# Kernel tuning notes

Measured on AMD Instinct MI355X. Metric: run time of the kernel, lower is better.

The kernel has to match this reference:

```python
import jax, jax.numpy as jnp
import numpy as np

BLOCK, HALO, HEADS, DH = 8, 4, 4, 32
EPS = 1e-5


def _convT(x, w, p):
    # torch ConvTranspose2d(stride=1, padding=p) == conv with flipped/transposed kernel, padding k-1-p
    k = w.shape[-1]
    w2 = jnp.flip(w, axis=(-2, -1)).transpose(1, 0, 2, 3)  # (Cin,Cout,k,k) -> (Cout,Cin,k,k)
    pad = k - 1 - p
    return jax.lax.conv_general_dilated(x, w2, (1, 1), ((pad, pad), (pad, pad)),
                                        dimension_numbers=('NCHW', 'OIHW', 'NCHW'))


def _bn(x, g, b, m, v):
    s = g * jax.lax.rsqrt(v + EPS)
    return x * s[None, :, None, None] + (b - m * s)[None, :, None, None]


def _rel_to_abs(x):
    # x: [b, l, 2r-1] -> [b, l, r]
    b, l, m = x.shape
    r = (m + 1) // 2
    x = jnp.concatenate([x, jnp.zeros((b, l, 1), x.dtype)], axis=2)
    flat = jnp.concatenate([x.reshape(b, l * (m + 1)), jnp.zeros((b, m - l), x.dtype)], axis=1)
    return flat.reshape(b, l + 1, m)[:, :l, -r:]


def _rel_logits_1d(q, rel_k):
    # q: [b, x, y, d]; rel_k: [2r-1, d] -> [b, x, r, y, r]
    b, x, y, d = q.shape
    r = (rel_k.shape[0] + 1) // 2
    logits = jnp.einsum('bxyd,rd->bxyr', q, rel_k)
    logits = _rel_to_abs(logits.reshape(b * x, y, -1)).reshape(b, x, y, r)
    return jnp.broadcast_to(logits[:, :, None, :, :], (b, x, r, y, r))


def _rel_pos_emb(q, rel_h, rel_w):
    # q: [bb, block*block, dh] (already scaled, per halonet-pytorch)
    bb, n, d = q.shape
    qg = q.reshape(bb, BLOCK, BLOCK, d)
    lw = _rel_logits_1d(qg, rel_w).transpose(0, 1, 3, 2, 4).reshape(bb, n, -1)  # b (x y) (i j)
    lh = _rel_logits_1d(qg.transpose(0, 2, 1, 3), rel_h).transpose(0, 3, 1, 4, 2).reshape(bb, n, -1)  # b (y x) (j i)
    return lw + lh


def _halo_attn(x, to_q, to_kv, to_out_w, to_out_b, rel_h, rel_w):
    B, C, H, W = x.shape
    b, h = BLOCK, HALO
    nh, nw = H // b, W // b
    nblk = nh * nw
    wsz = b + 2 * h
    inner = to_q.shape[1]
    scale = DH ** -0.5
    # queries: non-overlapping blocks -> [B*nblk, b*b, C]
    q_inp = x.reshape(B, C, nh, b, nw, b).transpose(0, 2, 4, 3, 5, 1).reshape(B * nblk, b * b, C)
    # keys/values: overlapping halo windows (F.unfold) -> [B*nblk, wsz*wsz, C]
    pat = jax.lax.conv_general_dilated_patches(x, (wsz, wsz), (b, b), ((h, h), (h, h)))  # [B, C*wsz*wsz, nh, nw]
    kv_inp = pat.reshape(B, C, wsz * wsz, nblk).transpose(0, 3, 2, 1).reshape(B * nblk, wsz * wsz, C)
    q = q_inp @ to_q
    k, v = jnp.split(kv_inp @ to_kv, 2, axis=-1)
    def heads(t):
        return t.reshape(t.shape[0], t.shape[1], HEADS, DH).transpose(0, 2, 1, 3).reshape(-1, t.shape[1], DH)
    q, k, v = heads(q) * scale, heads(k), heads(v)
    sim = jnp.einsum('bid,bjd->bij', q, k) + _rel_pos_emb(q, rel_h, rel_w)  # [B*nblk*HEADS, b*b, wsz*wsz]
    # mask out halo positions that fall into zero padding
    ones = jnp.ones((1, 1, H, W), x.dtype)
    mpat = jax.lax.conv_general_dilated_patches(ones, (wsz, wsz), (b, b), ((h, h), (h, h)))
    mask = mpat.reshape(wsz * wsz, nblk).T > 0  # [nblk, wsz*wsz]
    neg = -jnp.finfo(sim.dtype).max
    sim = jnp.where(mask[None, :, None, None, :],
                    sim.reshape(B, nblk, HEADS, b * b, wsz * wsz), neg)
    attn = jax.nn.softmax(sim, axis=-1).reshape(-1, b * b, wsz * wsz)
    out = jnp.einsum('bij,bjd->bid', attn, v)
    out = out.reshape(B * nblk, HEADS, b * b, DH).transpose(0, 2, 1, 3).reshape(B * nblk, b * b, inner)
    out = out @ to_out_w + to_out_b
    return out.reshape(B, nh, nw, b, b, C).transpose(0, 5, 1, 3, 2, 4).reshape(B, C, H, W)


def setup_inputs() -> dict:
    key = jax.random.key(0)
    ks = jax.random.split(key, 13)
    B, C, H, W = 2, 128, 192, 192
    inner = HEADS * DH
    rel = 2 * (BLOCK + 2 * HALO) - 1  # 31
    n = lambda k, s, sc: jax.random.normal(k, s, jnp.float32) * sc
    return {
        'x': jax.random.normal(ks[0], (B, C, H, W), jnp.float32),
        'conv1_w': n(ks[1], (C, C, 1, 1), 0.1),
        'bn1_g': jnp.ones((C,), jnp.float32), 'bn1_b': jnp.zeros((C,), jnp.float32),
        'bn1_m': n(ks[2], (C,), 0.1),
        'bn1_v': jax.random.uniform(ks[3], (C,), jnp.float32, 0.5, 1.5),
        'to_q': n(ks[4], (C, inner), 0.05), 'to_kv': n(ks[5], (C, 2 * inner), 0.05),
        'to_out_w': n(ks[6], (inner, C), 0.05), 'to_out_b': n(ks[7], (C,), 0.01),
        'rel_h': n(ks[8], (rel, DH), DH ** -0.5), 'rel_w': n(ks[9], (rel, DH), DH ** -0.5),
        'conv3_w': n(ks[10], (C, C, 3, 3), 0.05),
        'bn3_g': jnp.ones((C,), jnp.float32), 'bn3_b': jnp.zeros((C,), jnp.float32),
        'bn3_m': n(ks[11], (C,), 0.1),
        'bn3_v': jax.random.uniform(ks[12], (C,), jnp.float32, 0.5, 1.5),
    }


def reference(x, conv1_w, bn1_g, bn1_b, bn1_m, bn1_v, to_q, to_kv, to_out_w, to_out_b,
              rel_h, rel_w, conv3_w, bn3_g, bn3_b, bn3_m, bn3_v):
    # Bottleneck (stride=1, no downsample): conv1x1T -> BN -> ReLU -> HaloAttention -> ReLU
    #   -> conv3x3T -> BN -> +identity -> ReLU
    out = jax.nn.relu(_bn(_convT(x, conv1_w, 0), bn1_g, bn1_b, bn1_m, bn1_v))
    out = jax.nn.relu(_halo_attn(out, to_q, to_kv, to_out_w, to_out_b, rel_h, rel_w))
    out = _bn(_convT(out, conv3_w, 1), bn3_g, bn3_b, bn3_m, bn3_v)
    return jax.nn.relu(out + x)
```

## Files before the change

kernel.cpp:

```cpp
#include <hip/hip_runtime.h>
#include <hip/hip_bf16.h>

using bf16 = __hip_bfloat16;
typedef unsigned short u16;
typedef unsigned int   u32;
typedef __attribute__((ext_vector_type(8))) short short8;
typedef __attribute__((ext_vector_type(4))) float f32x4;

#define B_N 2
#define CCH 128
#define HH 192
#define WW 192
#define HWS (HH*WW)
#define NPIX (B_N*HWS)
#define NBLKS 576
#define EPSV 1e-5f
#define LDW 136

__device__ __forceinline__ float b2f(bf16 v){ return __bfloat162float(v); }
__device__ __forceinline__ bf16  f2b(float v){ return __float2bfloat16(v); }
__device__ __forceinline__ u16  bits(bf16 v){ return *(u16*)&v; }
__device__ __forceinline__ float lo16(u32 u){ union{u32 i; float f;} x; x.i = u << 16;        return x.f; }
__device__ __forceinline__ float hi16(u32 u){ union{u32 i; float f;} x; x.i = u & 0xffff0000u; return x.f; }
__device__ __forceinline__ u32 pck(float a, float b){
    bf16 x = f2b(a), y = f2b(b);
    return (u32)*(u16*)&x | ((u32)*(u16*)&y << 16);
}

__global__ __launch_bounds__(256) void transpose_in(const float* __restrict__ x,
                                                    bf16* __restrict__ xT)
{
    __shared__ float tile[128][17];
    const int t   = threadIdx.x;
    const int hw0 = blockIdx.x * 16;
    const int n   = hw0 / HWS;
    const int hwl = hw0 - n*HWS;
    const int px = t & 15, cb = t >> 4;
    #pragma unroll
    for (int r = 0; r < 8; ++r){
        int ci = r*16 + cb;
        tile[ci][px] = x[(size_t)(n*CCH + ci)*HWS + hwl + px];
    }
    __syncthreads();
    const int pix = t >> 4, cig = t & 15;
    uint4 pk;
    pk.x = pck(tile[cig*8+0][pix], tile[cig*8+1][pix]);
    pk.y = pck(tile[cig*8+2][pix], tile[cig*8+3][pix]);
    pk.z = pck(tile[cig*8+4][pix], tile[cig*8+5][pix]);
    pk.w = pck(tile[cig*8+6][pix], tile[cig*8+7][pix]);
    *(uint4*)&xT[(size_t)(hw0 + pix)*CCH + cig*8] = pk;
}

__global__ __launch_bounds__(256) void prep_w(
    const float* __restrict__ w1, const float* __restrict__ to_q,
    const float* __restrict__ to_kv, const float* __restrict__ to_ow,
    const float* __restrict__ w3, bf16* __restrict__ wb)
{
    int i = blockIdx.x*256 + threadIdx.x;
    float v;
    if (i < 16384){       int co=(i>>7)&127, ci=i&127;      v = w1[ci*128+co]; }
    else if (i < 32768){  int r=i-16384; int co=r>>7, ci=r&127; v = to_q[ci*128+co]*0.17677669529663687f; }
    else if (i < 49152){  int r=i-32768; int co=r>>7, ci=r&127; v = to_kv[ci*256+co]; }
    else if (i < 65536){  int r=i-49152; int co=r>>7, ci=r&127; v = to_kv[ci*256+128+co]; }
    else if (i < 81920){  int r=i-65536; int co=r>>7, ci=r&127; v = to_ow[ci*128+co]; }
    else { int r=i-81920; int tap=r>>14, co=(r>>7)&127, ci=r&127; int a=tap/3, b=tap-a*3;
           v = w3[((size_t)(ci*128+co)*3+a)*3+b]; }
    wb[i] = f2b(v);
}

template<bool DO_BN, bool DO_BIAS, bool DO_RELU>
__global__ __launch_bounds__(256) void gemm_mfma(
    const bf16* __restrict__ inp, const bf16* __restrict__ Wp,
    bf16* __restrict__ outp, int cstride, int choff,
    const float* __restrict__ bn_g, const float* __restrict__ bn_b,
    const float* __restrict__ bn_m, const float* __restrict__ bn_v,
    const float* __restrict__ bias)
{
    Wp    += (size_t)blockIdx.y * 16384;
    choff += blockIdx.y * 128;
    __shared__ u16 sW[128*LDW];
    __shared__ u16 sX[64*LDW];
    const int tid  = threadIdx.x;
    const int pix0 = blockIdx.x * 64;
    const int lane = tid & 63;
    const int ln = lane & 15, g = lane >> 4;
    const int cow = (tid >> 6) * 32;

    #pragma unroll
    for (int r = 0; r < 8; ++r){
        int e = tid + r*256; int row = e>>4, grp = e&15;
        *(uint4*)&sW[row*LDW + grp*8] = *(const uint4*)&Wp[row*128 + grp*8];
    }
    #pragma unroll
    for (int r = 0; r < 4; ++r){
        int e = tid + r*256; int row = e>>4, grp = e&15;
        *(uint4*)&sX[row*LDW + grp*8] = *(const uint4*)&inp[(size_t)(pix0+row)*CCH + grp*8];
    }
    __syncthreads();

    f32x4 acc[4][2];
    #pragma unroll
    for (int mi=0;mi<4;mi++)
        #pragma unroll
        for (int ni=0;ni<2;ni++) acc[mi][ni] = (f32x4){0.f,0.f,0.f,0.f};

    #pragma unroll
    for (int kk = 0; kk < 4; ++kk){
        short8 fa[4], fb[2];
        #pragma unroll
        for (int mi=0;mi<4;mi++)
            fa[mi] = *(const short8*)&sX[(mi*16+ln)*LDW + kk*32 + g*8];
        #pragma unroll
        for (int ni=0;ni<2;ni++)
            fb[ni] = *(const short8*)&sW[(cow+ni*16+ln)*LDW + kk*32 + g*8];
        #pragma unroll
        for (int mi=0;mi<4;mi++)
            #pragma unroll
            for (int ni=0;ni<2;ni++)
                acc[mi][ni] = __builtin_amdgcn_mfma_f32_16x16x32_bf16(fa[mi], fb[ni], acc[mi][ni], 0, 0, 0);
    }

    float sc[2], bb[2];
    #pragma unroll
    for (int ni=0;ni<2;ni++){
        int co = cow + ni*16 + ln;
        sc[ni] = 1.f; bb[ni] = 0.f;
        if (DO_BN){ float sg = bn_g[co]*rsqrtf(bn_v[co]+EPSV); sc[ni]=sg; bb[ni]=bn_b[co]-bn_m[co]*sg; }
        if (DO_BIAS) bb[ni] += bias[co];
    }
    #pragma unroll
    for (int mi=0;mi<4;mi++)
        #pragma unroll
        for (int ni=0;ni<2;ni++)
            #pragma unroll
            for (int j=0;j<4;j++){
                int pix = pix0 + mi*16 + g*4 + j;
                int co  = cow + ni*16 + ln;
                float v = acc[mi][ni][j]*sc[ni] + bb[ni];
                if (DO_RELU) v = fmaxf(v, 0.f);
                outp[(size_t)pix*cstride + choff + co] = f2b(v);
            }
}

__global__ __launch_bounds__(256) void conv3_mfma(
    const bf16* __restrict__ inp, const bf16* __restrict__ W3p,
    const float* __restrict__ xin, float* __restrict__ outp,
    const float* __restrict__ g3, const float* __restrict__ b3,
    const float* __restrict__ m3, const float* __restrict__ v3)
{
    __shared__ u16 sW[128*LDW];
    __shared__ u16 sX[64*LDW];
    const int tid = threadIdx.x;
    const int P0  = blockIdx.x * 64;
    const int n   = P0 / HWS;
    const int hwb = P0 - n*HWS;
    const int h = hwb / WW, wb = hwb - h*WW;
    const int lane = tid & 63, ln = lane & 15, g = lane >> 4;
    const int cow = (tid >> 6) * 32;

    f32x4 acc[2][4];
    #pragma unroll
    for (int mi=0;mi<2;mi++)
        #pragma unroll
        for (int ni=0;ni<4;ni++) acc[mi][ni] = (f32x4){0.f,0.f,0.f,0.f};

    for (int tap = 0; tap < 9; ++tap){
        const int a = tap/3, b = tap - a*3;
        const int hs = h + 1 - a;
        if (hs < 0 || hs >= HH) continue;
        const int ws0 = wb + 1 - b;
        __syncthreads();
        #pragma unroll
        for (int r = 0; r < 8; ++r){
            int e = tid + r*256; int row = e>>4, grp = e&15;
            *(uint4*)&sW[row*LDW + grp*8] = *(const uint4*)&W3p[tap*16384 + row*128 + grp*8];
        }
        #pragma unroll
        for (int r = 0; r < 4; ++r){
            int e = tid + r*256; int row = e>>4, grp = e&15;
            int wsrc = ws0 + row;
            uint4 val = {0u,0u,0u,0u};
            if (wsrc >= 0 && wsrc < WW)
                val = *(const uint4*)&inp[(size_t)(n*HWS + hs*WW + wsrc)*CCH + grp*8];
            *(uint4*)&sX[row*LDW + grp*8] = val;
        }
        __syncthreads();
        #pragma unroll
        for (int kk = 0; kk < 4; ++kk){
            short8 fa[2], fb[4];
            #pragma unroll
            for (int mi=0;mi<2;mi++)
                fa[mi] = *(const short8*)&sW[(cow+mi*16+ln)*LDW + kk*32 + g*8];
            #pragma unroll
            for (int ni=0;ni<4;ni++)
                fb[ni] = *(const short8*)&sX[(ni*16+ln)*LDW + kk*32 + g*8];
            #pragma unroll
            for (int mi=0;mi<2;mi++)
                #pragma unroll
                for (int ni=0;ni<4;ni++)
                    acc[mi][ni] = __builtin_amdgcn_mfma_f32_16x16x32_bf16(fa[mi], fb[ni], acc[mi][ni], 0, 0, 0);
        }
    }

    #pragma unroll
    for (int mi=0;mi<2;mi++)
        #pragma unroll
        for (int j=0;j<4;j++){
            int co = cow + mi*16 + g*4 + j;
            float sg = g3[co]*rsqrtf(v3[co]+EPSV);
            float bc = b3[co] - m3[co]*sg;
            #pragma unroll
            for (int ni=0;ni<4;ni++){
                int pixl = hwb + ni*16 + ln;
                size_t idx = (size_t)(n*CCH + co)*HWS + pixl;
                float v = acc[mi][ni][j]*sg + bc + xin[idx];
                outp[idx] = fmaxf(v, 0.f);
            }
        }
}

__global__ __launch_bounds__(512) void attn_kernel(
    const bf16* __restrict__ QKV, const float* __restrict__ relh,
    const float* __restrict__ relw, bf16* __restrict__ outp)
{
    __shared__ __align__(16) char smem[60160];
    u16*   sQb  = (u16*)(smem);
    u16*   sK   = (u16*)(smem + 5120);
    u16*   sRH  = (u16*)(smem + 25600);
    u16*   sRW  = (u16*)(smem + 28160);
    u16*   sP   = (u16*)(smem);
    u16*   sVT  = (u16*)(smem + 33792);
    float* tT   = (float*)(smem + 50688);
    float* wredM= (float*)(smem + 59136);
    float* wredS= (float*)(smem + 59648);

    const int tid  = threadIdx.x;
    const int bid  = blockIdx.x;
    const int head = bid & 3;
    const int t    = bid >> 2;
    const int n    = t / NBLKS;
    const int blk  = t - n*NBLKS;
    const int bi = blk / 24, bj = blk - bi*24;
    const int row0 = bi*8 - 4, col0 = bj*8 - 4;
    const int ch0 = head*32;
    const int wv = tid >> 6, lane = tid & 63, ln = lane & 15, g = lane >> 4;
    const int nt = wv & 3, mh = wv >> 2;

    for (int e = tid; e < 1024; e += 512){
        int r = e >> 5, d = e & 31;
        u16 vh = 0, vw = 0;
        if (r < 31){ vh = bits(f2b(relh[r*32+d])); vw = bits(f2b(relw[r*32+d])); }
        sRH[r*40 + d] = vh;
        sRW[r*40 + d] = vw;
    }
    {
        int qq = tid >> 3, db = tid & 7;
        size_t P = (size_t)n*HWS + (bi*8 + (qq>>3))*WW + bj*8 + (qq&7);
        *(uint2*)&sQb[qq*40 + db*4] = *(const uint2*)&QKV[P*384 + ch0 + db*4];
    }
    #pragma unroll
    for (int r = 0; r < 4; ++r){
        int e = tid + r*512;
        int wp = e >> 3, db = e & 7;
        int rr = row0 + (wp>>4), cc2 = col0 + (wp&15);
        uint2 kk = {0u,0u}, vv = {0u,0u};
        if (rr>=0 && rr<HH && cc2>=0 && cc2<WW){
            size_t P = (size_t)n*HWS + rr*WW + cc2;
            kk = *(const uint2*)&QKV[P*384 + 128 + ch0 + db*4];
            vv = *(const uint2*)&QKV[P*384 + 256 + ch0 + db*4];
        }
        *(uint2*)&sK[wp*40 + db*4] = kk;
        sVT[(db*4+0)*264 + wp] = (u16)(vv.x & 0xffff);
        sVT[(db*4+1)*264 + wp] = (u16)(vv.x >> 16);
        sVT[(db*4+2)*264 + wp] = (u16)(vv.y & 0xffff);
        sVT[(db*4+3)*264 + wp] = (u16)(vv.y >> 16);
    }
    __syncthreads();

    const short8 qfrag = *(const short8*)&sQb[(nt*16+ln)*40 + g*8];
    f32x4 accs[8];
    #pragma unroll
    for (int i=0;i<8;i++){
        short8 fk = *(const short8*)&sK[((mh*8+i)*16+ln)*40 + g*8];
        accs[i] = __builtin_amdgcn_mfma_f32_16x16x32_bf16(fk, qfrag, (f32x4){0.f,0.f,0.f,0.f}, 0, 0, 0);
    }

    {
        const u16* sRX = mh ? sRW : sRH;
        #pragma unroll
        for (int ntr=0; ntr<2; ++ntr){
            short8 fr = *(const short8*)&sRX[(ntr*16+ln)*40 + g*8];
            f32x4 L = __builtin_amdgcn_mfma_f32_16x16x32_bf16(qfrag, fr, (f32x4){0.f,0.f,0.f,0.f}, 0, 0, 0);
            #pragma unroll
            for (int r2=0;r2<4;r2++){
                int q  = nt*16 + g*4 + r2;
                int rr = ntr*16 + ln;
                int bq = mh ? (q&7) : (q>>3);
                int iw = rr - 15 + bq;
                if (iw >= 0 && iw < 16) tT[mh*1056 + iw*66 + q] = L[r2];
            }
        }
    }
    __syncthreads();

    const int qc = nt*16 + ln;
    float tw[4];
    bool cok[4];
    #pragma unroll
    for (int r2=0;r2<4;r2++){
        tw[r2] = tT[1056 + (g*4+r2)*66 + qc];
        int cc2 = col0 + g*4 + r2;
        cok[r2] = (cc2 >= 0 && cc2 < WW);
    }
    float mx = -3.4e38f;
    #pragma unroll
    for (int i=0;i<8;i++){
        int mt = mh*8 + i;
        int rr = row0 + mt;
        bool rok = (rr >= 0 && rr < HH);
        float th = tT[mt*66 + qc];
        #pragma unroll
        for (int r2=0;r2<4;r2++){
            float s = (rok && cok[r2]) ? (accs[i][r2] + th + tw[r2]) : -3.0e38f;
            accs[i][r2] = s;
            mx = fmaxf(mx, s);
        }
    }
    mx = fmaxf(mx, __shfl_xor(mx, 16));
    mx = fmaxf(mx, __shfl_xor(mx, 32));
    if (g == 0) wredM[mh*64 + qc] = mx;
    __syncthreads();
    mx = fmaxf(wredM[qc], wredM[64 + qc]);

    float sm = 0.f;
    #pragma unroll
    for (int i=0;i<8;i++){
        int mt = mh*8 + i;
        float p0 = __expf(accs[i][0]-mx);
        float p1 = __expf(accs[i][1]-mx);
        float p2 = __expf(accs[i][2]-mx);
        float p3 = __expf(accs[i][3]-mx);
        sm += (p0+p1)+(p2+p3);
        u32* dst = (u32*)&sP[qc*264 + mt*16 + g*4];
        dst[0] = pck(p0,p1);
        dst[1] = pck(p2,p3);
    }
    sm += __shfl_xor(sm, 16);
    sm += __shfl_xor(sm, 32);
    if (g == 0) wredS[mh*64 + qc] = sm;
    __syncthreads();

    const int mtPV = wv >> 1, ntPV = wv & 1;
    f32x4 acco = (f32x4){0.f,0.f,0.f,0.f};
    #pragma unroll
    for (int ks=0; ks<8; ++ks){
        short8 fp = *(const short8*)&sP [(mtPV*16+ln)*264 + ks*32 + g*8];
        short8 fv = *(const short8*)&sVT[(ntPV*16+ln)*264 + ks*32 + g*8];
        acco = __builtin_amdgcn_mfma_f32_16x16x32_bf16(fp, fv, acco, 0, 0, 0);
    }
    const int d = ntPV*16 + ln;
    #pragma unroll
    for (int r2=0;r2<4;r2++){
        int qq = mtPV*16 + g*4 + r2;
        float inv = 1.f / (wredS[qq] + wredS[64 + qq]);
        size_t P = (size_t)n*HWS + (bi*8 + (qq>>3))*WW + bj*8 + (qq&7);
        outp[P*CCH + ch0 + d] = f2b(acco[r2] * inv);
    }
}

extern "C" void kernel_launch(void* const* d_in, const int* in_sizes, int n_in,
                              void* d_out, int out_size, void* d_ws, size_t ws_size,
                              hipStream_t stream)
{
    (void)in_sizes; (void)n_in; (void)out_size; (void)ws_size;
    const float* x      = (const float*)d_in[0];
    const float* w1     = (const float*)d_in[1];
    const float* bn1_g  = (const float*)d_in[2];
    const float* bn1_b  = (const float*)d_in[3];
    const float* bn1_m  = (const float*)d_in[4];
    const float* bn1_v  = (const float*)d_in[5];
    const float* to_q   = (const float*)d_in[6];
    const float* to_kv  = (const float*)d_in[7];
    const float* to_ow  = (const float*)d_in[8];
    const float* to_ob  = (const float*)d_in[9];
    const float* rel_h  = (const float*)d_in[10];
    const float* rel_w  = (const float*)d_in[11];
    const float* w3     = (const float*)d_in[12];
    const float* bn3_g  = (const float*)d_in[13];
    const float* bn3_b  = (const float*)d_in[14];
    const float* bn3_m  = (const float*)d_in[15];
    const float* bn3_v  = (const float*)d_in[16];

    char* ws   = (char*)d_ws;
    bf16* out1 = (bf16*)(ws + 0);
    bf16* qkv  = (bf16*)(ws + 18874368);
    bf16* xT   = (bf16*)(ws + 75497472);
    bf16* wb   = (bf16*)(ws + 94371840);
    bf16* W3p  = wb + 81920;
    bf16* attnout = (bf16*)d_out;
    bf16* out2    = out1;

    transpose_in<<<4608, 256, 0, stream>>>(x, xT);
    prep_w<<<896, 256, 0, stream>>>(w1, to_q, to_kv, to_ow, w3, wb);

    gemm_mfma<true,false,true><<<dim3(1152,1), 256, 0, stream>>>(
        xT, wb, out1, 128, 0, bn1_g, bn1_b, bn1_m, bn1_v, nullptr);
    gemm_mfma<false,false,false><<<dim3(1152,3), 256, 0, stream>>>(
        out1, wb + 16384, qkv, 384, 0, nullptr,nullptr,nullptr,nullptr,nullptr);

    attn_kernel<<<4608, 512, 0, stream>>>(qkv, rel_h, rel_w, attnout);

    gemm_mfma<false,true,true><<<dim3(1152,1), 256, 0, stream>>>(
        attnout, wb + 65536, out2, 128, 0, nullptr,nullptr,nullptr,nullptr, to_ob);

    conv3_mfma<<<1152, 256, 0, stream>>>(out2, W3p, x, (float*)d_out,
                                         bn3_g, bn3_b, bn3_m, bn3_v);
}
```

Measured before the change: 177.6 us.

## Write V projection channel-major so attention loads V^T with vector reads

The V projection now runs as a separate GEMM variant that transposes its output tile through shared memory and stores V channel-major (NCHW), while Q and K remain pixel-major in a 256-wide buffer. The attention kernel then fills its transposed V shared tile with 8-byte row loads instead of scattered 2-byte LDS writes per element. The attention block index is also remapped to interleave blocks across groups, presumably for cache or XCD locality. This costs an extra kernel launch and an LDS transpose pass in the GEMM, and adds a halo-column boundary check.

```diff
diff --git a/kernel.cpp b/kernel.cpp
--- a/kernel.cpp
+++ b/kernel.cpp
@@ -20,8 +20,6 @@
 __device__ __forceinline__ float b2f(bf16 v){ return __bfloat162float(v); }
 __device__ __forceinline__ bf16  f2b(float v){ return __float2bfloat16(v); }
 __device__ __forceinline__ u16  bits(bf16 v){ return *(u16*)&v; }
-__device__ __forceinline__ float lo16(u32 u){ union{u32 i; float f;} x; x.i = u << 16;        return x.f; }
-__device__ __forceinline__ float hi16(u32 u){ union{u32 i; float f;} x; x.i = u & 0xffff0000u; return x.f; }
 __device__ __forceinline__ u32 pck(float a, float b){
     bf16 x = f2b(a), y = f2b(b);
     return (u32)*(u16*)&x | ((u32)*(u16*)&y << 16);
@@ -68,7 +66,7 @@
     wb[i] = f2b(v);
 }
 
-template<bool DO_BN, bool DO_BIAS, bool DO_RELU>
+template<bool DO_BN, bool DO_BIAS, bool DO_RELU, bool OUT_TRANS>
 __global__ __launch_bounds__(256) void gemm_mfma(
     const bf16* __restrict__ inp, const bf16* __restrict__ Wp,
     bf16* __restrict__ outp, int cstride, int choff,
@@ -120,6 +118,29 @@
                 acc[mi][ni] = __builtin_amdgcn_mfma_f32_16x16x32_bf16(fa[mi], fb[ni], acc[mi][ni], 0, 0, 0);
     }
 
+    if (OUT_TRANS){
+        __syncthreads();
+        u16* tile = sX;
+        #pragma unroll
+        for (int mi=0;mi<4;mi++)
+            #pragma unroll
+            for (int ni=0;ni<2;ni++){
+                int co   = cow + ni*16 + ln;
+                int pixl = mi*16 + g*4;
+                *(u32*)&tile[co*68 + pixl]     = pck(acc[mi][ni][0], acc[mi][ni][1]);
+                *(u32*)&tile[co*68 + pixl + 2] = pck(acc[mi][ni][2], acc[mi][ni][3]);
+            }
+        __syncthreads();
+        const int co2 = tid >> 1, hf = tid & 1;
+        const int n2 = pix0 / HWS, hwb2 = pix0 - n2*HWS;
+        u16* gdst = (u16*)outp + (size_t)(n2*CCH + co2)*HWS + hwb2 + hf*32;
+        const u16* src = &tile[co2*68 + hf*32];
+        #pragma unroll
+        for (int k=0;k<8;k++)
+            *(uint2*)&gdst[k*4] = *(const uint2*)&src[k*4];
+        return;
+    }
+
     float sc[2], bb[2];
     #pragma unroll
     for (int ni=0;ni<2;ni++){
@@ -220,8 +241,9 @@
 }
 
 __global__ __launch_bounds__(512) void attn_kernel(
-    const bf16* __restrict__ QKV, const float* __restrict__ relh,
-    const float* __restrict__ relw, bf16* __restrict__ outp)
+    const u16* __restrict__ QK, const u16* __restrict__ vT,
+    const float* __restrict__ relh, const float* __restrict__ relw,
+    bf16* __restrict__ outp)
 {
     __shared__ __align__(16) char smem[60160];
     u16*   sQb  = (u16*)(smem);
@@ -235,7 +257,8 @@
     float* wredS= (float*)(smem + 59648);
 
     const int tid  = threadIdx.x;
-    const int bid  = blockIdx.x;
+    const int bid0 = blockIdx.x;
+    const int bid  = (bid0 & 7) * 576 + (bid0 >> 3);
     const int head = bid & 3;
     const int t    = bid >> 2;
     const int n    = t / NBLKS;
@@ -256,24 +279,32 @@
     {
         int qq = tid >> 3, db = tid & 7;
         size_t P = (size_t)n*HWS + (bi*8 + (qq>>3))*WW + bj*8 + (qq&7);
-        *(uint2*)&sQb[qq*40 + db*4] = *(const uint2*)&QKV[P*384 + ch0 + db*4];
+        *(uint2*)&sQb[qq*40 + db*4] = *(const uint2*)&QK[P*256 + ch0 + db*4];
     }
     #pragma unroll
     for (int r = 0; r < 4; ++r){
         int e = tid + r*512;
         int wp = e >> 3, db = e & 7;
         int rr = row0 + (wp>>4), cc2 = col0 + (wp&15);
-        uint2 kk = {0u,0u}, vv = {0u,0u};
+        uint2 kk2 = {0u,0u};
         if (rr>=0 && rr<HH && cc2>=0 && cc2<WW){
             size_t P = (size_t)n*HWS + rr*WW + cc2;
-            kk = *(const uint2*)&QKV[P*384 + 128 + ch0 + db*4];
-            vv = *(const uint2*)&QKV[P*384 + 256 + ch0 + db*4];
-        }
-        *(uint2*)&sK[wp*40 + db*4] = kk;
-        sVT[(db*4+0)*264 + wp] = (u16)(vv.x & 0xffff);
-        sVT[(db*4+1)*264 + wp] = (u16)(vv.x >> 16);
-        sVT[(db*4+2)*264 + wp] = (u16)(vv.y & 0xffff);
-        sVT[(db*4+3)*264 + wp] = (u16)(vv.y >> 16);
+            kk2 = *(const uint2*)&QK[P*256 + 128 + ch0 + db*4];
+        }
+        *(uint2*)&sK[wp*40 + db*4] = kk2;
+    }
+    #pragma unroll
+    for (int r = 0; r < 4; ++r){
+        int e = tid + r*512;
+        int d   = e >> 6;
+        int rem = e & 63;
+        int iw  = rem >> 2;
+        int jc  = (rem & 3) * 4;
+        int rr  = row0 + iw, cc0 = col0 + jc;
+        uint2 vv = {0u,0u};
+        if (rr >= 0 && rr < HH && cc0 >= 0 && cc0 < 189)
+            vv = *(const uint2*)&vT[(size_t)(n*CCH + ch0 + d)*HWS + rr*WW + cc0];
+        *(uint2*)&sVT[d*264 + iw*16 + jc] = vv;
     }
     __syncthreads();
 
@@ -393,8 +424,9 @@
 
     char* ws   = (char*)d_ws;
     bf16* out1 = (bf16*)(ws + 0);
-    bf16* qkv  = (bf16*)(ws + 18874368);
-    bf16* xT   = (bf16*)(ws + 75497472);
+    bf16* qk   = (bf16*)(ws + 18874368);
+    bf16* xT   = (bf16*)(ws + 56623104);
+    bf16* vT   = (bf16*)(ws + 75497472);
     bf16* wb   = (bf16*)(ws + 94371840);
     bf16* W3p  = wb + 81920;
     bf16* attnout = (bf16*)d_out;
@@ -403,14 +435,17 @@
     transpose_in<<<4608, 256, 0, stream>>>(x, xT);
     prep_w<<<896, 256, 0, stream>>>(w1, to_q, to_kv, to_ow, w3, wb);
 
-    gemm_mfma<true,false,true><<<dim3(1152,1), 256, 0, stream>>>(
+    gemm_mfma<true,false,true,false><<<dim3(1152,1), 256, 0, stream>>>(
         xT, wb, out1, 128, 0, bn1_g, bn1_b, bn1_m, bn1_v, nullptr);
-    gemm_mfma<false,false,false><<<dim3(1152,3), 256, 0, stream>>>(
-        out1, wb + 16384, qkv, 384, 0, nullptr,nullptr,nullptr,nullptr,nullptr);
-
-    attn_kernel<<<4608, 512, 0, stream>>>(qkv, rel_h, rel_w, attnout);
-
-    gemm_mfma<false,true,true><<<dim3(1152,1), 256, 0, stream>>>(
+    gemm_mfma<false,false,false,false><<<dim3(1152,2), 256, 0, stream>>>(
+        out1, wb + 16384, qk, 256, 0, nullptr,nullptr,nullptr,nullptr,nullptr);
+    gemm_mfma<false,false,false,true><<<dim3(1152,1), 256, 0, stream>>>(
+        out1, wb + 49152, vT, 0, 0, nullptr,nullptr,nullptr,nullptr,nullptr);
+
+    attn_kernel<<<4608, 512, 0, stream>>>((const u16*)qk, (const u16*)vT,
+                                          rel_h, rel_w, attnout);
+
+    gemm_mfma<false,true,true,false><<<dim3(1152,1), 256, 0, stream>>>(
         attnout, wb + 65536, out2, 128, 0, nullptr,nullptr,nullptr,nullptr, to_ob);
 
     conv3_mfma<<<1152, 256, 0, stream>>>(out2, W3p, x, (float*)d_out,
```

Result: slower. 189.3 us (+6.6%).
